# Performance work log

Measured on AMD Instinct MI355X. Metric: run time of the kernel, lower is better.

Reference implementation:

```python
import jax, jax.numpy as jnp
import numpy as np

N_NODES = 100000
N_EDGES = 1600000
N_PAIRS = 200000
IN_CH = 128
HID_CH = 128


def _graph_conv(x, src, dst, edge_weight, w_rel, b_rel, w_root, num_nodes):
    # PyG GraphConv with aggr='mean':
    # out = lin_rel(mean_{j in N(i)}(x_j * w_ij)) + lin_root(x_i)
    msg = x[src] * edge_weight[:, None]                       # [E, C] gather
    agg = jax.ops.segment_sum(msg, dst, num_segments=num_nodes)  # [N, C]
    cnt = jax.ops.segment_sum(jnp.ones((src.shape[0],), x.dtype), dst,
                              num_segments=num_nodes)          # in-degree
    agg = agg / jnp.maximum(cnt, 1.0)[:, None]                 # mean aggr
    return agg @ w_rel + b_rel + x @ w_root


def setup_inputs() -> dict:
    key = jax.random.key(0)
    ks = jax.random.split(key, 10)
    x = jax.random.normal(ks[0], (N_NODES, IN_CH), dtype=jnp.float32)
    edge_index = jax.random.randint(ks[1], (2, N_EDGES), 0, N_NODES, dtype=jnp.int32)
    edge_weight = jax.random.uniform(ks[2], (N_EDGES,), dtype=jnp.float32)
    edge_label_index = jax.random.randint(ks[3], (2, N_PAIRS), 0, N_NODES, dtype=jnp.int32)
    s1 = 1.0 / np.sqrt(IN_CH)
    s2 = 1.0 / np.sqrt(HID_CH)
    w1_rel = jax.random.uniform(ks[4], (IN_CH, HID_CH), jnp.float32, -s1, s1)
    b1_rel = jnp.zeros((HID_CH,), jnp.float32)
    w1_root = jax.random.uniform(ks[5], (IN_CH, HID_CH), jnp.float32, -s1, s1)
    w2_rel = jax.random.uniform(ks[6], (HID_CH, HID_CH), jnp.float32, -s2, s2)
    b2_rel = jnp.zeros((HID_CH,), jnp.float32)
    w2_root = jax.random.uniform(ks[7], (HID_CH, HID_CH), jnp.float32, -s2, s2)
    return {"x": x, "edge_index": edge_index, "edge_weight": edge_weight,
            "edge_label_index": edge_label_index,
            "w1_rel": w1_rel, "b1_rel": b1_rel, "w1_root": w1_root,
            "w2_rel": w2_rel, "b2_rel": b2_rel, "w2_root": w2_root}


def reference(x, edge_index, edge_weight, edge_label_index,
              w1_rel, b1_rel, w1_root, w2_rel, b2_rel, w2_root):
    src, dst = edge_index[0], edge_index[1]
    # encode
    h = _graph_conv(x, src, dst, edge_weight, w1_rel, b1_rel, w1_root, x.shape[0])
    h = jax.nn.relu(h)
    z = _graph_conv(h, src, dst, edge_weight, w2_rel, b2_rel, w2_root, x.shape[0])
    # decode: scaled dot product between candidate pair embeddings
    zs = z[edge_label_index[0]]   # [P, H]
    zd = z[edge_label_index[1]]   # [P, H]
    scale = z.shape[-1] ** 0.5
    return jnp.sum(zs * zd, axis=-1) / scale
```

## Files before the change

kernel.cpp:

```cpp
#include <hip/hip_runtime.h>

#define NN 100000
#define NE 1600000
#define NP 200000
#define CH 128
#define SB 1024
#define LK 264
#define CPAD 16

typedef _Float16 f16x8 __attribute__((ext_vector_type(8)));
typedef _Float16 f16x2 __attribute__((ext_vector_type(2)));
typedef float f32x4 __attribute__((ext_vector_type(4)));

__global__ void cast_kernel(const float* __restrict__ in, _Float16* __restrict__ out, int n8) {
    int i = blockIdx.x * blockDim.x + threadIdx.x;
    if (i >= n8) return;
    const float4* p = (const float4*)in + (size_t)i * 2;
    float4 a = p[0], b = p[1];
    f16x8 o = { (_Float16)a.x, (_Float16)a.y, (_Float16)a.z, (_Float16)a.w,
                (_Float16)b.x, (_Float16)b.y, (_Float16)b.z, (_Float16)b.w };
    *((f16x8*)out + i) = o;
}

__global__ void count_rank_kernel(const int* __restrict__ dst, int* __restrict__ cnt,
                                  int* __restrict__ rank, int E) {
    int t = blockIdx.x * blockDim.x + threadIdx.x;
    int e0 = t * 8;
    if (e0 >= E) return;
    int4 d0 = *(const int4*)&dst[e0];
    int4 d1 = *(const int4*)&dst[e0 + 4];
    int4 r0, r1;
    r0.x = atomicAdd(&cnt[d0.x * CPAD], 1);
    r0.y = atomicAdd(&cnt[d0.y * CPAD], 1);
    r0.z = atomicAdd(&cnt[d0.z * CPAD], 1);
    r0.w = atomicAdd(&cnt[d0.w * CPAD], 1);
    r1.x = atomicAdd(&cnt[d1.x * CPAD], 1);
    r1.y = atomicAdd(&cnt[d1.y * CPAD], 1);
    r1.z = atomicAdd(&cnt[d1.z * CPAD], 1);
    r1.w = atomicAdd(&cnt[d1.w * CPAD], 1);
    *(int4*)&rank[e0] = r0;
    *(int4*)&rank[e0 + 4] = r1;
}

__global__ __launch_bounds__(SB)
void scan1_kernel(const int* __restrict__ cnt, int* __restrict__ row_ptr,
                  int* __restrict__ partials, int n) {
    __shared__ int s[SB];
    int i = blockIdx.x * SB + threadIdx.x;
    int v = (i < n) ? cnt[i * CPAD] : 0;
    s[threadIdx.x] = v;
    __syncthreads();
    for (int off = 1; off < SB; off <<= 1) {
        int t = (threadIdx.x >= off) ? s[threadIdx.x - off] : 0;
        __syncthreads();
        s[threadIdx.x] += t;
        __syncthreads();
    }
    if (i < n) row_ptr[i + 1] = s[threadIdx.x];
    if (threadIdx.x == SB - 1) partials[blockIdx.x] = s[SB - 1];
}

__global__ __launch_bounds__(128)
void scan2_kernel(int* __restrict__ partials, int nb) {
    __shared__ int s[128];
    int v = (threadIdx.x < nb) ? partials[threadIdx.x] : 0;
    s[threadIdx.x] = v;
    __syncthreads();
    for (int off = 1; off < 128; off <<= 1) {
        int t = (threadIdx.x >= off) ? s[threadIdx.x - off] : 0;
        __syncthreads();
        s[threadIdx.x] += t;
        __syncthreads();
    }
    if (threadIdx.x < nb) partials[threadIdx.x] = s[threadIdx.x];
}

__global__ __launch_bounds__(SB)
void scan3_kernel(int* __restrict__ row_ptr, const int* __restrict__ partials, int n) {
    int i = blockIdx.x * SB + threadIdx.x;
    if (i < n && blockIdx.x > 0) row_ptr[i + 1] += partials[blockIdx.x - 1];
    if (i == 0) row_ptr[0] = 0;
}

__global__ void fill_kernel(const int* __restrict__ src, const int* __restrict__ dst,
                            const float* __restrict__ ew, const int* __restrict__ row_ptr,
                            const int* __restrict__ rank, int2* __restrict__ csr, int E) {
    int e = blockIdx.x * blockDim.x + threadIdx.x;
    if (e >= E) return;
    int pos = row_ptr[dst[e]] + rank[e];
    csr[pos] = make_int2(src[e], __float_as_int(ew[e]));
}

__global__ __launch_bounds__(256)
void gather_kernel(const _Float16* __restrict__ feat, const int* __restrict__ row_ptr,
                   const int2* __restrict__ csr, _Float16* __restrict__ agg, int N) {
    int node = blockIdx.x * 4 + (threadIdx.x >> 6);
    if (node >= N) return;
    int lane = threadIdx.x & 63;
    int q = lane >> 4;
    int l16 = lane & 15;
    int c8 = l16 << 3;
    int r0 = row_ptr[node], r1 = row_ptr[node + 1];
    float acc[8] = {0.f, 0.f, 0.f, 0.f, 0.f, 0.f, 0.f, 0.f};
    int r = r0 + q;
    if (r < r1) {
        int2 e = csr[r];
        f16x8 v = *(const f16x8*)&feat[(size_t)e.x * CH + c8];
        for (r += 4; r < r1; r += 4) {
            int2 e2 = csr[r];
            f16x8 v2 = *(const f16x8*)&feat[(size_t)e2.x * CH + c8];
            float w = __int_as_float(e.y);
#pragma unroll
            for (int j = 0; j < 8; j++) acc[j] += w * (float)v[j];
            e = e2; v = v2;
        }
        float w = __int_as_float(e.y);
#pragma unroll
        for (int j = 0; j < 8; j++) acc[j] += w * (float)v[j];
    }
#pragma unroll
    for (int j = 0; j < 8; j++) {
        acc[j] += __shfl_xor(acc[j], 16, 64);
        acc[j] += __shfl_xor(acc[j], 32, 64);
    }
    if (q == 0) {
        float inv = 1.0f / fmaxf((float)(r1 - r0), 1.0f);
        f16x8 o;
#pragma unroll
        for (int j = 0; j < 8; j++) o[j] = (_Float16)(acc[j] * inv);
        *(f16x8*)&agg[(size_t)node * CH + c8] = o;
    }
}

__global__ void prep_w_kernel(const float* __restrict__ wr, const float* __restrict__ wo,
                              _Float16* __restrict__ wt) {
    int idx = blockIdx.x * 256 + threadIdx.x;
    if (idx >= 128 * 256) return;
    int n = idx >> 8, k = idx & 255;
    float v = (k < 128) ? wr[k * 128 + n] : wo[(k - 128) * 128 + n];
    wt[idx] = (_Float16)v;
}

template <bool RELU>
__global__ __launch_bounds__(256)
void layer_mfma_kernel(const _Float16* __restrict__ agg,
                       const _Float16* __restrict__ xin,
                       const _Float16* __restrict__ wt,
                       const float* __restrict__ bias,
                       _Float16* __restrict__ out, int N) {
    __shared__ _Float16 s_a[64][LK];

    const int tid = threadIdx.x;
    const int nb = blockIdx.x * 64;

    for (int i = tid; i < 64 * 32; i += 256) {
        int r = i >> 5;
        int c8 = (i & 31) << 3;
        int gn = nb + r;
        f16x8 v = {};
        if (gn < N) {
            const _Float16* srcp = (c8 < 128) ? &agg[(size_t)gn * CH + c8]
                                              : &xin[(size_t)gn * CH + (c8 - 128)];
            v = *(const f16x8*)srcp;
        }
        *(f16x8*)&s_a[r][c8] = v;
    }
    __syncthreads();

    const int wave = tid >> 6;
    const int lane = tid & 63;
    const int quad = lane >> 4;
    const int l16  = lane & 15;

    f32x4 acc[4][2];
#pragma unroll
    for (int m = 0; m < 4; m++)
#pragma unroll
        for (int t = 0; t < 2; t++) acc[m][t] = (f32x4){0.f, 0.f, 0.f, 0.f};

    const int kq = quad * 8;

#pragma unroll
    for (int ks = 0; ks < 8; ks++) {
        int kbase = ks * 32 + kq;
        f16x8 bf[2];
#pragma unroll
        for (int t = 0; t < 2; t++) {
            int n = wave * 32 + t * 16 + l16;
            bf[t] = *(const f16x8*)&wt[(size_t)n * 256 + kbase];
        }
#pragma unroll
        for (int m = 0; m < 4; m++) {
            f16x8 af = *(const f16x8*)&s_a[m * 16 + l16][kbase];
            acc[m][0] = __builtin_amdgcn_mfma_f32_16x16x32_f16(af, bf[0], acc[m][0], 0, 0, 0);
            acc[m][1] = __builtin_amdgcn_mfma_f32_16x16x32_f16(af, bf[1], acc[m][1], 0, 0, 0);
        }
    }

    float bv[2];
    bv[0] = bias[wave * 32 + l16];
    bv[1] = bias[wave * 32 + 16 + l16];

#pragma unroll
    for (int m = 0; m < 4; m++) {
#pragma unroll
        for (int r = 0; r < 4; r++) {
            int node = nb + m * 16 + quad * 4 + r;
            if (node >= N) continue;
#pragma unroll
            for (int t = 0; t < 2; t++) {
                float v = acc[m][t][r] + bv[t];
                if (RELU) v = fmaxf(v, 0.f);
                out[(size_t)node * CH + wave * 32 + t * 16 + l16] = (_Float16)v;
            }
        }
    }
}

__global__ void decode_kernel(const _Float16* __restrict__ z,
                              const int* __restrict__ ps,
                              const int* __restrict__ pd,
                              float* __restrict__ out, int P) {
    long tid = (long)blockIdx.x * blockDim.x + threadIdx.x;
    int p = (int)(tid >> 6);
    int lane = (int)(tid & 63);
    if (p >= P) return;
    int s = ps[p], d = pd[p];
    f16x2 a = *(const f16x2*)&z[(size_t)s * CH + lane * 2];
    f16x2 b = *(const f16x2*)&z[(size_t)d * CH + lane * 2];
    float v = (float)a[0] * (float)b[0] + (float)a[1] * (float)b[1];
#pragma unroll
    for (int off = 32; off > 0; off >>= 1) v += __shfl_down(v, off, 64);
    if (lane == 0) out[p] = v * 0.08838834764831845f;
}

extern "C" void kernel_launch(void* const* d_in, const int* in_sizes, int n_in,
                              void* d_out, int out_size, void* d_ws, size_t ws_size,
                              hipStream_t stream) {
    const float* x       = (const float*)d_in[0];
    const int*   ei      = (const int*)d_in[1];
    const float* ew      = (const float*)d_in[2];
    const int*   eli     = (const int*)d_in[3];
    const float* w1_rel  = (const float*)d_in[4];
    const float* b1      = (const float*)d_in[5];
    const float* w1_root = (const float*)d_in[6];
    const float* w2_rel  = (const float*)d_in[7];
    const float* b2      = (const float*)d_in[8];
    const float* w2_root = (const float*)d_in[9];
    float* out = (float*)d_out;

    const int N = NN, E = NE, P = NP;
    const size_t hrow = (size_t)N * CH * sizeof(_Float16);

    char* ws = (char*)d_ws;
    size_t off = 0;
    auto alloc = [&](size_t bytes) { char* p = ws + off; off = (off + bytes + 15) & ~(size_t)15; return p; };
    _Float16* xh   = (_Float16*)alloc(hrow);
    _Float16* aggh = (_Float16*)alloc(hrow);
    _Float16* hh   = (_Float16*)alloc(hrow);
    _Float16* zh   = aggh;
    int* cnt      = (int*)alloc((size_t)N * CPAD * 4);
    int* row_ptr  = (int*)alloc((size_t)(N + 1) * 4);
    int* partials = (int*)alloc(256 * 4);
    int* rank     = (int*)alloc((size_t)E * 4);
    int2* csr     = (int2*)alloc((size_t)E * 8);
    _Float16* w1t = (_Float16*)alloc((size_t)128 * 256 * 2);
    _Float16* w2t = (_Float16*)alloc((size_t)128 * 256 * 2);

    const int* src = ei;
    const int* dst = ei + E;

    const int nb_scan = (N + SB - 1) / SB;
    const int n8 = N * CH / 8;

    cast_kernel<<<(n8 + 255) / 256, 256, 0, stream>>>(x, xh, n8);
    prep_w_kernel<<<128, 256, 0, stream>>>(w1_rel, w1_root, w1t);
    prep_w_kernel<<<128, 256, 0, stream>>>(w2_rel, w2_root, w2t);

    hipMemsetAsync(cnt, 0, (size_t)N * CPAD * 4, stream);
    {
        int nthr = E / 8;
        count_rank_kernel<<<(nthr + 255) / 256, 256, 0, stream>>>(dst, cnt, rank, E);
    }
    scan1_kernel<<<nb_scan, SB, 0, stream>>>(cnt, row_ptr, partials, N);
    scan2_kernel<<<1, 128, 0, stream>>>(partials, nb_scan);
    scan3_kernel<<<nb_scan, SB, 0, stream>>>(row_ptr, partials, N);
    fill_kernel<<<(E + 255) / 256, 256, 0, stream>>>(src, dst, ew, row_ptr, rank, csr, E);

    gather_kernel<<<(N + 3) / 4, 256, 0, stream>>>(xh, row_ptr, csr, aggh, N);
    layer_mfma_kernel<true><<<(N + 63) / 64, 256, 0, stream>>>(aggh, xh, w1t, b1, hh, N);

    gather_kernel<<<(N + 3) / 4, 256, 0, stream>>>(hh, row_ptr, csr, aggh, N);
    layer_mfma_kernel<false><<<(N + 63) / 64, 256, 0, stream>>>(aggh, hh, w2t, b2, zh, N);

    {
        long threads = (long)P * 64;
        decode_kernel<<<(int)((threads + 255) / 256), 256, 0, stream>>>(zh, eli, eli + P, out, P);
    }
}
```

Measured before the change: 439.8 us.

## Build CSR with two-level bucket sort instead of global atomic counting

Replaces the per-node global atomic count, rank and scan CSR construction with a two-pass bucketed counting sort. Edges are first histogrammed and scattered into buckets of 64 destination nodes using shared-memory atomics, then each bucket is sorted locally in LDS to produce row_ptr and the CSR. The aim is to remove contended global atomics and the random scatter into a padded counter array. In exchange it adds an extra edge buffer, more kernel launches, and a serial column scan over 256 histogram rows.

```diff
diff --git a/kernel.cpp b/kernel.cpp
--- a/kernel.cpp
+++ b/kernel.cpp
@@ -4,9 +4,13 @@
 #define NE 1600000
 #define NP 200000
 #define CH 128
-#define SB 1024
 #define LK 264
-#define CPAD 16
+
+#define BSH 6
+#define NB  1563
+#define G1  256
+#define EPB (NE / G1)
+#define CAP3 4096
 
 typedef _Float16 f16x8 __attribute__((ext_vector_type(8)));
 typedef _Float16 f16x2 __attribute__((ext_vector_type(2)));
@@ -22,73 +26,116 @@
     *((f16x8*)out + i) = o;
 }
 
-__global__ void count_rank_kernel(const int* __restrict__ dst, int* __restrict__ cnt,
-                                  int* __restrict__ rank, int E) {
-    int t = blockIdx.x * blockDim.x + threadIdx.x;
-    int e0 = t * 8;
-    if (e0 >= E) return;
-    int4 d0 = *(const int4*)&dst[e0];
-    int4 d1 = *(const int4*)&dst[e0 + 4];
-    int4 r0, r1;
-    r0.x = atomicAdd(&cnt[d0.x * CPAD], 1);
-    r0.y = atomicAdd(&cnt[d0.y * CPAD], 1);
-    r0.z = atomicAdd(&cnt[d0.z * CPAD], 1);
-    r0.w = atomicAdd(&cnt[d0.w * CPAD], 1);
-    r1.x = atomicAdd(&cnt[d1.x * CPAD], 1);
-    r1.y = atomicAdd(&cnt[d1.y * CPAD], 1);
-    r1.z = atomicAdd(&cnt[d1.z * CPAD], 1);
-    r1.w = atomicAdd(&cnt[d1.w * CPAD], 1);
-    *(int4*)&rank[e0] = r0;
-    *(int4*)&rank[e0 + 4] = r1;
-}
-
-__global__ __launch_bounds__(SB)
-void scan1_kernel(const int* __restrict__ cnt, int* __restrict__ row_ptr,
-                  int* __restrict__ partials, int n) {
-    __shared__ int s[SB];
-    int i = blockIdx.x * SB + threadIdx.x;
-    int v = (i < n) ? cnt[i * CPAD] : 0;
-    s[threadIdx.x] = v;
-    __syncthreads();
-    for (int off = 1; off < SB; off <<= 1) {
-        int t = (threadIdx.x >= off) ? s[threadIdx.x - off] : 0;
+__global__ __launch_bounds__(256)
+void bucket_hist_kernel(const int* __restrict__ dst, int* __restrict__ hist ) {
+    __shared__ int s_h[NB];
+    for (int i = threadIdx.x; i < NB; i += 256) s_h[i] = 0;
+    __syncthreads();
+    int start = blockIdx.x * EPB, end = start + EPB;
+    for (int e = start + threadIdx.x; e < end; e += 256)
+        atomicAdd(&s_h[dst[e] >> BSH], 1);
+    __syncthreads();
+    int* row = hist + (size_t)blockIdx.x * NB;
+    for (int i = threadIdx.x; i < NB; i += 256) row[i] = s_h[i];
+}
+
+__global__ void colscan_kernel(int* __restrict__ hist, int* __restrict__ totals) {
+    int b = blockIdx.x * blockDim.x + threadIdx.x;
+    if (b >= NB) return;
+    int run = 0;
+    for (int g = 0; g < G1; g++) {
+        size_t idx = (size_t)g * NB + b;
+        int v = hist[idx];
+        hist[idx] = run;
+        run += v;
+    }
+    totals[b] = run;
+}
+
+__global__ __launch_bounds__(1024)
+void scanB_kernel(const int* __restrict__ totals, int* __restrict__ base) {
+    __shared__ int s[2048];
+    int tid = threadIdx.x;
+    for (int i = tid; i < 2048; i += 1024) s[i] = (i < NB) ? totals[i] : 0;
+    __syncthreads();
+    for (int off = 1; off < 2048; off <<= 1) {
+        int i0 = tid, i1 = tid + 1024;
+        int v0 = (i0 >= off) ? s[i0 - off] : 0;
+        int v1 = (i1 >= off) ? s[i1 - off] : 0;
         __syncthreads();
-        s[threadIdx.x] += t;
+        s[i0] += v0; s[i1] += v1;
         __syncthreads();
     }
-    if (i < n) row_ptr[i + 1] = s[threadIdx.x];
-    if (threadIdx.x == SB - 1) partials[blockIdx.x] = s[SB - 1];
-}
-
-__global__ __launch_bounds__(128)
-void scan2_kernel(int* __restrict__ partials, int nb) {
-    __shared__ int s[128];
-    int v = (threadIdx.x < nb) ? partials[threadIdx.x] : 0;
-    s[threadIdx.x] = v;
-    __syncthreads();
-    for (int off = 1; off < 128; off <<= 1) {
-        int t = (threadIdx.x >= off) ? s[threadIdx.x - off] : 0;
-        __syncthreads();
-        s[threadIdx.x] += t;
-        __syncthreads();
-    }
-    if (threadIdx.x < nb) partials[threadIdx.x] = s[threadIdx.x];
-}
-
-__global__ __launch_bounds__(SB)
-void scan3_kernel(int* __restrict__ row_ptr, const int* __restrict__ partials, int n) {
-    int i = blockIdx.x * SB + threadIdx.x;
-    if (i < n && blockIdx.x > 0) row_ptr[i + 1] += partials[blockIdx.x - 1];
-    if (i == 0) row_ptr[0] = 0;
-}
-
-__global__ void fill_kernel(const int* __restrict__ src, const int* __restrict__ dst,
-                            const float* __restrict__ ew, const int* __restrict__ row_ptr,
-                            const int* __restrict__ rank, int2* __restrict__ csr, int E) {
-    int e = blockIdx.x * blockDim.x + threadIdx.x;
-    if (e >= E) return;
-    int pos = row_ptr[dst[e]] + rank[e];
-    csr[pos] = make_int2(src[e], __float_as_int(ew[e]));
+    if (tid == 0) base[0] = 0;
+    for (int i = tid; i < NB; i += 1024) base[i + 1] = s[i];
+}
+
+__global__ __launch_bounds__(256)
+void bucket_scatter_kernel(const int* __restrict__ src, const int* __restrict__ dst,
+                           const float* __restrict__ ew, const int* __restrict__ hist,
+                           const int* __restrict__ base, int2* __restrict__ tmp) {
+    __shared__ int s_cur[NB];
+    const int* row = hist + (size_t)blockIdx.x * NB;
+    for (int i = threadIdx.x; i < NB; i += 256) s_cur[i] = base[i] + row[i];
+    __syncthreads();
+    int start = blockIdx.x * EPB, end = start + EPB;
+    for (int e = start + threadIdx.x; e < end; e += 256) {
+        int d = dst[e];
+        int b = d >> BSH;
+        int pos = atomicAdd(&s_cur[b], 1);
+        tmp[pos] = make_int2(src[e] | ((d & 63) << 17), __float_as_int(ew[e]));
+    }
+}
+
+__global__ __launch_bounds__(256)
+void bucket_finalize_kernel(const int2* __restrict__ tmp, const int* __restrict__ base,
+                            int* __restrict__ row_ptr, int2* __restrict__ csr, int N) {
+    __shared__ int2 s_e[CAP3];
+    __shared__ int s_cnt[64], s_off[64];
+    int b = blockIdx.x;
+    int lo = base[b], hi = base[b + 1];
+    int size = hi - lo;
+    int nbase = b << BSH;
+    int ncnt = min(64, N - nbase);
+    int tid = threadIdx.x;
+    if (tid < 64) s_cnt[tid] = 0;
+    bool inlds = (size <= CAP3);
+    __syncthreads();
+    if (inlds) {
+        for (int i = tid; i < size; i += 256) {
+            int2 e = tmp[lo + i];
+            s_e[i] = e;
+            atomicAdd(&s_cnt[(e.x >> 17) & 63], 1);
+        }
+    } else {
+        for (int i = tid; i < size; i += 256) {
+            int2 e = tmp[lo + i];
+            atomicAdd(&s_cnt[(e.x >> 17) & 63], 1);
+        }
+    }
+    __syncthreads();
+    if (tid == 0) {
+        int run = 0;
+        for (int i = 0; i < 64; i++) { int v = s_cnt[i]; s_off[i] = run; s_cnt[i] = run; run += v; }
+    }
+    __syncthreads();
+    if (tid < ncnt) row_ptr[nbase + tid] = lo + s_off[tid];
+    if (b == NB - 1 && tid == 0) row_ptr[N] = hi;
+    if (inlds) {
+        for (int i = tid; i < size; i += 256) {
+            int2 e = s_e[i];
+            int dl = (e.x >> 17) & 63;
+            int p = atomicAdd(&s_cnt[dl], 1);
+            csr[lo + p] = make_int2(e.x & 0x1FFFF, e.y);
+        }
+    } else {
+        for (int i = tid; i < size; i += 256) {
+            int2 e = tmp[lo + i];
+            int dl = (e.x >> 17) & 63;
+            int p = atomicAdd(&s_cnt[dl], 1);
+            csr[lo + p] = make_int2(e.x & 0x1FFFF, e.y);
+        }
+    }
 }
 
 __global__ __launch_bounds__(256)
@@ -259,10 +306,11 @@
     _Float16* aggh = (_Float16*)alloc(hrow);
     _Float16* hh   = (_Float16*)alloc(hrow);
     _Float16* zh   = aggh;
-    int* cnt      = (int*)alloc((size_t)N * CPAD * 4);
+    int* hist     = (int*)alloc((size_t)G1 * NB * 4);
+    int* totals   = (int*)alloc((size_t)NB * 4);
+    int* base     = (int*)alloc((size_t)(NB + 1) * 4);
     int* row_ptr  = (int*)alloc((size_t)(N + 1) * 4);
-    int* partials = (int*)alloc(256 * 4);
-    int* rank     = (int*)alloc((size_t)E * 4);
+    int2* tmp     = (int2*)alloc((size_t)E * 8);
     int2* csr     = (int2*)alloc((size_t)E * 8);
     _Float16* w1t = (_Float16*)alloc((size_t)128 * 256 * 2);
     _Float16* w2t = (_Float16*)alloc((size_t)128 * 256 * 2);
@@ -270,22 +318,17 @@
     const int* src = ei;
     const int* dst = ei + E;
 
-    const int nb_scan = (N + SB - 1) / SB;
     const int n8 = N * CH / 8;
 
     cast_kernel<<<(n8 + 255) / 256, 256, 0, stream>>>(x, xh, n8);
     prep_w_kernel<<<128, 256, 0, stream>>>(w1_rel, w1_root, w1t);
     prep_w_kernel<<<128, 256, 0, stream>>>(w2_rel, w2_root, w2t);
 
-    hipMemsetAsync(cnt, 0, (size_t)N * CPAD * 4, stream);
-    {
-        int nthr = E / 8;
-        count_rank_kernel<<<(nthr + 255) / 256, 256, 0, stream>>>(dst, cnt, rank, E);
-    }
-    scan1_kernel<<<nb_scan, SB, 0, stream>>>(cnt, row_ptr, partials, N);
-    scan2_kernel<<<1, 128, 0, stream>>>(partials, nb_scan);
-    scan3_kernel<<<nb_scan, SB, 0, stream>>>(row_ptr, partials, N);
-    fill_kernel<<<(E + 255) / 256, 256, 0, stream>>>(src, dst, ew, row_ptr, rank, csr, E);
+    bucket_hist_kernel<<<G1, 256, 0, stream>>>(dst, hist);
+    colscan_kernel<<<(NB + 255) / 256, 256, 0, stream>>>(hist, totals);
+    scanB_kernel<<<1, 1024, 0, stream>>>(totals, base);
+    bucket_scatter_kernel<<<G1, 256, 0, stream>>>(src, dst, ew, hist, base, tmp);
+    bucket_finalize_kernel<<<NB, 256, 0, stream>>>(tmp, base, row_ptr, csr, N);
 
     gather_kernel<<<(N + 3) / 4, 256, 0, stream>>>(xh, row_ptr, csr, aggh, N);
     layer_mfma_kernel<true><<<(N + 63) / 64, 256, 0, stream>>>(aggh, xh, w1t, b1, hh, N);
```

Result: faster. 410.3 us (-6.7%).
